# Optimization experiments

Measured on AMD Instinct MI355X. Metric: run time of the kernel, lower is better.

Reference implementation:

```python
import jax, jax.numpy as jnp
import numpy as np

EPS = 1e-8
VOX_WIDTH = 1.0
CURV_THRESH = 0.5


def _build_kernels():
    """Nine 3x3x3 central finite-difference stencils, pre-divided by vox_width / vox_width^2."""
    def zk():
        return np.zeros((3, 3, 3), np.float32)
    ks = {}
    # first derivatives (central difference), denominator vox_width
    for name, ax in (('ddx', 0), ('ddy', 1), ('ddz', 2)):
        k = zk(); i = [1, 1, 1]
        i[ax] = 0; k[tuple(i)] = -0.5
        i[ax] = 2; k[tuple(i)] = 0.5
        ks[name] = k / VOX_WIDTH
    # pure second derivatives, denominator vox_width^2
    for name, ax in (('d2dx2', 0), ('d2dy2', 1), ('d2dz2', 2)):
        k = zk(); i = [1, 1, 1]
        i[ax] = 0; k[tuple(i)] = 1.0
        i[ax] = 1; k[tuple(i)] = -2.0
        i[ax] = 2; k[tuple(i)] = 1.0
        ks[name] = k / VOX_WIDTH ** 2
    # mixed second derivatives, denominator vox_width^2
    for name, (a, b) in (('d2dxdy', (0, 1)), ('d2dxdz', (0, 2)), ('d2dydz', (1, 2))):
        k = zk()
        for sa, sb, v in ((0, 0, 0.25), (0, 2, -0.25), (2, 0, -0.25), (2, 2, 0.25)):
            i = [1, 1, 1]; i[a] = sa; i[b] = sb; k[tuple(i)] = v
        ks[name] = k / VOX_WIDTH ** 2
    order = ['ddx', 'ddy', 'ddz', 'd2dx2', 'd2dy2', 'd2dz2', 'd2dxdy', 'd2dxdz', 'd2dydz']
    return np.stack([ks[n] for n in order])[:, None]  # [9, 1, 3, 3, 3]


_KERNELS = jnp.asarray(_build_kernels())


def setup_inputs() -> dict:
    key = jax.random.key(0)
    phi = jax.random.normal(key, (2, 1, 192, 192, 192), dtype=jnp.float32)
    return {"phi": phi}


def reference(phi):
    # all nine stencils as one valid 3D conv: [N, 9, D-2, H-2, W-2]
    g = jax.lax.conv_general_dilated(
        phi, _KERNELS, window_strides=(1, 1, 1), padding='VALID',
        dimension_numbers=('NCDHW', 'OIDHW', 'NCDHW'))
    gx, gy, gz, hxx, hyy, hzz, hxy, hxz, hyz = (g[:, i:i + 1] for i in range(9))

    mag = jnp.sqrt(gx * gx + gy * gy + gz * gz + EPS)
    mag3 = mag ** 3

    # mean curvature: sum_{i!=j} g_i^2 H_jj - 2 sum_{i<j} g_i g_j H_ij, over |grad|^3
    cross = gx * gy * hxy + gx * gz * hxz + gy * gz * hyz
    mean_c = (gx * gx * (hyy + hzz) + gy * gy * (hxx + hzz) + gz * gz * (hxx + hyy)
              - 2.0 * cross) / (mag3 + EPS)

    # gaussian curvature: laplacian/|grad| - (g^T H g)/|grad|^3
    lap = (hxx + hyy + hzz) / (mag + EPS)
    quad = (gx * gx * hxx + gy * gy * hyy + gz * gz * hzz + 2.0 * cross) / (mag3 + EPS)
    gauss = lap - quad

    k1 = mean_c + jnp.sqrt(jnp.abs(mean_c ** 2 - gauss) + EPS)
    pen = jax.nn.relu((k1 / (CURV_THRESH + EPS)) ** 2 - 1.0)

    # zero crossings of phi over 3x3x3 neighborhoods (valid -> matches conv output shape)
    mn = jax.lax.reduce_window(phi, jnp.inf, jax.lax.min, (1, 1, 3, 3, 3), (1, 1, 1, 1, 1), 'VALID')
    mx = jax.lax.reduce_window(phi, -jnp.inf, jax.lax.max, (1, 1, 3, 3, 3), (1, 1, 1, 1, 1), 'VALID')
    phi_zero = jax.lax.stop_gradient((mn * mx < 0).astype(phi.dtype))

    return jnp.sum(phi_zero * pen) / (jnp.sum(phi_zero) + EPS)
```

## Files before the change

### kernel.cpp

```cpp
#include <hip/hip_runtime.h>


typedef float v2f __attribute__((ext_vector_type(2)));

constexpr int DIM  = 192;
constexpr int ODIM = 190;
constexpr int TX = 32, TY = 32, CZ = 19;
constexpr int NTX = 6, NTY = 6, NTZ = 10;
constexpr int PLANE = DIM * DIM;
constexpr int NBLOCKS = 2 * NTZ * NTY * NTX;

struct Slice {
    v2f   q[3][4];
    float xmn[4], xmx[4];
};

__global__ __launch_bounds__(256, 3) void curv_main(const float* __restrict__ phi,
                                                    double* __restrict__ acc,
                                                    int use_partials) {
    int bx = blockIdx.x;
    const int tx = bx % NTX; bx /= NTX;
    const int ty = bx % NTY; bx /= NTY;
    const int tz = bx % NTZ; bx /= NTZ;
    const int n  = bx;

    const int xbase = tx * TX, ybase = ty * TY, zbase = tz * CZ;
    const int tid = threadIdx.x;
    const int row = tid >> 3;
    const int x0  = (tid & 7) * 4;
    const float* pn = phi + (long long)n * DIM * PLANE;

    const int c4 = xbase + x0;
    int c2t = c4 + 4; if (c2t > DIM - 2) c2t = DIM - 2;
    const int c2 = c2t;
    int yoff[3];
#pragma unroll
    for (int dy = 0; dy < 3; ++dy) {
        int iy = ybase + row + dy; if (iy > DIM - 1) iy = DIM - 1;
        yoff[dy] = iy * DIM;
    }

    float4 t4[3]; float2 t2[3];
    auto pref = [&](int g) {
        const float* base = pn + (zbase + g) * PLANE;
#pragma unroll
        for (int dy = 0; dy < 3; ++dy) {
            t4[dy] = *(const float4*)(base + yoff[dy] + c4);
            t2[dy] = *(const float2*)(base + yoff[dy] + c2);
        }
    };

    auto unpack = [&](Slice& s) {
        float mn6[6], mx6[6];
#pragma unroll
        for (int dy = 0; dy < 3; ++dy) {
            const float4 a = t4[dy]; const float2 b = t2[dy];
            s.q[dy][0] = (v2f){a.x, a.z};
            s.q[dy][1] = (v2f){a.y, a.w};
            s.q[dy][2] = (v2f){a.z, b.x};
            s.q[dy][3] = (v2f){a.w, b.y};
            if (dy == 0) {
                mn6[0] = a.x; mn6[1] = a.y; mn6[2] = a.z;
                mn6[3] = a.w; mn6[4] = b.x; mn6[5] = b.y;
                mx6[0] = a.x; mx6[1] = a.y; mx6[2] = a.z;
                mx6[3] = a.w; mx6[4] = b.x; mx6[5] = b.y;
            } else {
                mn6[0] = fminf(mn6[0], a.x); mx6[0] = fmaxf(mx6[0], a.x);
                mn6[1] = fminf(mn6[1], a.y); mx6[1] = fmaxf(mx6[1], a.y);
                mn6[2] = fminf(mn6[2], a.z); mx6[2] = fmaxf(mx6[2], a.z);
                mn6[3] = fminf(mn6[3], a.w); mx6[3] = fmaxf(mx6[3], a.w);
                mn6[4] = fminf(mn6[4], b.x); mx6[4] = fmaxf(mx6[4], b.x);
                mn6[5] = fminf(mn6[5], b.y); mx6[5] = fmaxf(mx6[5], b.y);
            }
        }
#pragma unroll
        for (int j = 0; j < 4; ++j) {
            s.xmn[j] = fminf(fminf(mn6[j], mn6[j + 1]), mn6[j + 2]);
            s.xmx[j] = fmaxf(fmaxf(mx6[j], mx6[j + 1]), mx6[j + 2]);
        }
    };

    float fsp = 0.0f, fsc = 0.0f;
    const float EPSF = 1e-8f;
    const float EPS4 = 4e-8f;
    const int oy = ybase + row;

    bool vmask[4];
#pragma unroll
    for (int j = 0; j < 4; ++j)
        vmask[j] = (oy < ODIM) && (xbase + x0 + j < ODIM);

    auto compute = [&](const Slice& s0, const Slice& s1, const Slice& s2) {
        float wmn[4], wmx[4];
#pragma unroll
        for (int j = 0; j < 4; ++j) {
            wmn[j] = fminf(fminf(s0.xmn[j], s1.xmn[j]), s2.xmn[j]);
            wmx[j] = fmaxf(fmaxf(s0.xmx[j], s1.xmx[j]), s2.xmx[j]);
        }

#pragma unroll
        for (int p = 0; p < 2; ++p) {
            v2f Gx = s2.q[1][p + 1] - s0.q[1][p + 1];
            v2f Gy = s1.q[2][p + 1] - s1.q[0][p + 1];
            v2f Gz = s1.q[1][p + 2] - s1.q[1][p];

            v2f c2v = 2.0f * s1.q[1][p + 1];
            v2f hxx = s0.q[1][p + 1] - c2v + s2.q[1][p + 1];
            v2f hyy = s1.q[0][p + 1] - c2v + s1.q[2][p + 1];
            v2f hzz = s1.q[1][p] - c2v + s1.q[1][p + 2];

            v2f Mxy = s0.q[0][p + 1] - s0.q[2][p + 1]
                    - s2.q[0][p + 1] + s2.q[2][p + 1];
            v2f Mxz = s0.q[1][p] - s0.q[1][p + 2]
                    - s2.q[1][p] + s2.q[1][p + 2];
            v2f Myz = s1.q[0][p] - s1.q[0][p + 2]
                    - s1.q[2][p] + s1.q[2][p + 2];

            v2f Gx2 = Gx * Gx, Gy2 = Gy * Gy, Gz2 = Gz * Gz;
            v2f mag2G = Gx2 + Gy2 + Gz2 + EPS4;

            v2f r = (v2f){ __builtin_amdgcn_rsqf(mag2G.x),
                           __builtin_amdgcn_rsqf(mag2G.y) };
            v2f r3 = r * r * r;
            v2f twor3 = r3 + r3;

            v2f crossG = Gx * Gy * Mxy + Gx * Gz * Mxz + Gy * Gz * Myz;

            v2f num1 = Gx2 * (hyy + hzz) + Gy2 * (hxx + hzz) +
                       Gz2 * (hxx + hyy) - 0.5f * crossG;
            v2f mean_c = num1 * twor3;
            v2f lap   = (hxx + hyy + hzz) * (r + r);
            v2f num2  = Gx2 * hxx + Gy2 * hyy + Gz2 * hzz + 0.5f * crossG;
            v2f quad  = num2 * twor3;
            v2f gauss = lap - quad;

            v2f disc = mean_c * mean_c - gauss;
            v2f sq = (v2f){ sqrtf(fabsf(disc.x) + EPSF),
                            sqrtf(fabsf(disc.y) + EPSF) };
            v2f k1 = mean_c + sq;
            v2f t  = 2.0f * k1;
            v2f pen2 = t * t - 1.0f;

#pragma unroll
            for (int e = 0; e < 2; ++e) {
                const int j = p + 2 * e;
                float pen = fmaxf(e ? pen2.y : pen2.x, 0.0f);
                if (vmask[j] && (wmn[j] * wmx[j] < 0.0f)) {
                    fsp += pen;
                    fsc += 1.0f;
                }
            }
        }
    };

    Slice s0, s1, s2;

    pref(0); unpack(s0);
    pref(1); unpack(s1);
    pref(2);

    unpack(s2); pref(3);  compute(s0, s1, s2);
    unpack(s0); pref(4);  compute(s1, s2, s0);
    unpack(s1); pref(5);  compute(s2, s0, s1);
    unpack(s2); pref(6);  compute(s0, s1, s2);
    unpack(s0); pref(7);  compute(s1, s2, s0);
    unpack(s1); pref(8);  compute(s2, s0, s1);
    unpack(s2); pref(9);  compute(s0, s1, s2);
    unpack(s0); pref(10); compute(s1, s2, s0);
    unpack(s1); pref(11); compute(s2, s0, s1);
    unpack(s2); pref(12); compute(s0, s1, s2);
    unpack(s0); pref(13); compute(s1, s2, s0);
    unpack(s1); pref(14); compute(s2, s0, s1);
    unpack(s2); pref(15); compute(s0, s1, s2);
    unpack(s0); pref(16); compute(s1, s2, s0);
    unpack(s1); pref(17); compute(s2, s0, s1);
    unpack(s2); pref(18); compute(s0, s1, s2);
    unpack(s0); pref(19); compute(s1, s2, s0);
    unpack(s1); pref(20); compute(s2, s0, s1);
    unpack(s2);           compute(s0, s1, s2);

    double sp = (double)fsp, sc = (double)fsc;
#pragma unroll
    for (int off = 32; off > 0; off >>= 1) {
        sp += __shfl_down(sp, off, 64);
        sc += __shfl_down(sc, off, 64);
    }

    __shared__ double lsp[4], lsc[4];
    const int wave = tid >> 6, lane = tid & 63;
    if (lane == 0) { lsp[wave] = sp; lsc[wave] = sc; }
    __syncthreads();
    if (tid == 0) {
        double tp = lsp[0] + lsp[1] + lsp[2] + lsp[3];
        double tc = lsc[0] + lsc[1] + lsc[2] + lsc[3];
        if (use_partials) {
            acc[2 * blockIdx.x]     = tp;
            acc[2 * blockIdx.x + 1] = tc;
        } else {
            atomicAdd(&acc[0], tp);
            atomicAdd(&acc[1], tc);
        }
    }
}

__global__ __launch_bounds__(256) void curv_reduce(const double* __restrict__ part,
                                                   int nblocks, int use_partials,
                                                   float* __restrict__ out) {
    double sp = 0.0, sc = 0.0;
    if (use_partials) {
        for (int i = threadIdx.x; i < nblocks; i += 256) {
            sp += part[2 * i];
            sc += part[2 * i + 1];
        }
    } else if (threadIdx.x == 0) {
        sp = part[0]; sc = part[1];
    }
#pragma unroll
    for (int off = 32; off > 0; off >>= 1) {
        sp += __shfl_down(sp, off, 64);
        sc += __shfl_down(sc, off, 64);
    }
    __shared__ double lsp[4], lsc[4];
    const int wave = threadIdx.x >> 6, lane = threadIdx.x & 63;
    if (lane == 0) { lsp[wave] = sp; lsc[wave] = sc; }
    __syncthreads();
    if (threadIdx.x == 0) {
        double tp = lsp[0] + lsp[1] + lsp[2] + lsp[3];
        double tc = lsc[0] + lsc[1] + lsc[2] + lsc[3];
        out[0] = (float)(tp / (tc + 1e-8));
    }
}

extern "C" void kernel_launch(void* const* d_in, const int* in_sizes, int n_in,
                              void* d_out, int out_size, void* d_ws, size_t ws_size,
                              hipStream_t stream) {
    const float* phi = (const float*)d_in[0];
    float* out = (float*)d_out;
    double* acc = (double*)d_ws;

    const int use_partials = (ws_size >= (size_t)(2 * NBLOCKS) * sizeof(double)) ? 1 : 0;
    if (!use_partials) {
        hipMemsetAsync(d_ws, 0, 2 * sizeof(double), stream);
    }

    curv_main<<<NBLOCKS, 256, 0, stream>>>(phi, acc, use_partials);
    curv_reduce<<<1, 256, 0, stream>>>(acc, NBLOCKS, use_partials, out);
}
```

Baseline: 108.4 us.

## Fuse final reduction via last-block ticket, double-buffer prefetch, compact slice registers

The separate reduction kernel is replaced by a last-block-done pattern: each block writes its partial, bumps an atomic ticket, and the final block reduces all partials and writes the output. Launching one fewer kernel removes the launch gap, but a memset for the ticket is added. Prefetch now uses two alternating register buffers, so loads are issued two z-planes ahead. Slice storage is compacted from 12 to 9 packed pairs per slice, rebuilding the shifted pairs on demand to cut register pressure.

```diff
diff --git a/kernel.cpp b/kernel.cpp
--- a/kernel.cpp
+++ b/kernel.cpp
@@ -10,14 +10,53 @@
 constexpr int PLANE = DIM * DIM;
 constexpr int NBLOCKS = 2 * NTZ * NTY * NTX;
 
+struct Row { v2f A, B, C; };
 struct Slice {
-    v2f   q[3][4];
+    Row   r[3];
     float xmn[4], xmx[4];
 };
 
+#define PREF(T4, T2, g) do {                                             \
+    const float* base_ = pn + (zbase + (g)) * PLANE;                     \
+    _Pragma("unroll")                                                    \
+    for (int dy = 0; dy < 3; ++dy) {                                     \
+        T4[dy] = *(const float4*)(base_ + yoff[dy] + c4);                \
+        T2[dy] = *(const float2*)(base_ + yoff[dy] + c2);                \
+    } } while (0)
+
+#define UNPACK(S, T4, T2) do {                                           \
+    float mn6[6], mx6[6];                                                \
+    _Pragma("unroll")                                                    \
+    for (int dy = 0; dy < 3; ++dy) {                                     \
+        const float4 a = T4[dy]; const float2 b = T2[dy];                \
+        (S).r[dy].A = (v2f){a.x, a.z};                                   \
+        (S).r[dy].B = (v2f){a.y, a.w};                                   \
+        (S).r[dy].C = (v2f){b.x, b.y};                                   \
+        if (dy == 0) {                                                   \
+            mn6[0] = a.x; mn6[1] = a.y; mn6[2] = a.z;                    \
+            mn6[3] = a.w; mn6[4] = b.x; mn6[5] = b.y;                    \
+            mx6[0] = a.x; mx6[1] = a.y; mx6[2] = a.z;                    \
+            mx6[3] = a.w; mx6[4] = b.x; mx6[5] = b.y;                    \
+        } else {                                                         \
+            mn6[0] = fminf(mn6[0], a.x); mx6[0] = fmaxf(mx6[0], a.x);    \
+            mn6[1] = fminf(mn6[1], a.y); mx6[1] = fmaxf(mx6[1], a.y);    \
+            mn6[2] = fminf(mn6[2], a.z); mx6[2] = fmaxf(mx6[2], a.z);    \
+            mn6[3] = fminf(mn6[3], a.w); mx6[3] = fmaxf(mx6[3], a.w);    \
+            mn6[4] = fminf(mn6[4], b.x); mx6[4] = fmaxf(mx6[4], b.x);    \
+            mn6[5] = fminf(mn6[5], b.y); mx6[5] = fmaxf(mx6[5], b.y);    \
+        }                                                                \
+    }                                                                    \
+    _Pragma("unroll")                                                    \
+    for (int j = 0; j < 4; ++j) {                                        \
+        (S).xmn[j] = fminf(fminf(mn6[j], mn6[j + 1]), mn6[j + 2]);       \
+        (S).xmx[j] = fmaxf(fmaxf(mx6[j], mx6[j + 1]), mx6[j + 2]);       \
+    } } while (0)
+
 __global__ __launch_bounds__(256, 3) void curv_main(const float* __restrict__ phi,
                                                     double* __restrict__ acc,
-                                                    int use_partials) {
+                                                    float* __restrict__ out,
+                                                    unsigned* __restrict__ ticket,
+                                                    int mode) {
     int bx = blockIdx.x;
     const int tx = bx % NTX; bx /= NTX;
     const int ty = bx % NTY; bx /= NTY;
@@ -40,45 +79,8 @@
         yoff[dy] = iy * DIM;
     }
 
-    float4 t4[3]; float2 t2[3];
-    auto pref = [&](int g) {
-        const float* base = pn + (zbase + g) * PLANE;
-#pragma unroll
-        for (int dy = 0; dy < 3; ++dy) {
-            t4[dy] = *(const float4*)(base + yoff[dy] + c4);
-            t2[dy] = *(const float2*)(base + yoff[dy] + c2);
-        }
-    };
-
-    auto unpack = [&](Slice& s) {
-        float mn6[6], mx6[6];
-#pragma unroll
-        for (int dy = 0; dy < 3; ++dy) {
-            const float4 a = t4[dy]; const float2 b = t2[dy];
-            s.q[dy][0] = (v2f){a.x, a.z};
-            s.q[dy][1] = (v2f){a.y, a.w};
-            s.q[dy][2] = (v2f){a.z, b.x};
-            s.q[dy][3] = (v2f){a.w, b.y};
-            if (dy == 0) {
-                mn6[0] = a.x; mn6[1] = a.y; mn6[2] = a.z;
-                mn6[3] = a.w; mn6[4] = b.x; mn6[5] = b.y;
-                mx6[0] = a.x; mx6[1] = a.y; mx6[2] = a.z;
-                mx6[3] = a.w; mx6[4] = b.x; mx6[5] = b.y;
-            } else {
-                mn6[0] = fminf(mn6[0], a.x); mx6[0] = fmaxf(mx6[0], a.x);
-                mn6[1] = fminf(mn6[1], a.y); mx6[1] = fmaxf(mx6[1], a.y);
-                mn6[2] = fminf(mn6[2], a.z); mx6[2] = fmaxf(mx6[2], a.z);
-                mn6[3] = fminf(mn6[3], a.w); mx6[3] = fmaxf(mx6[3], a.w);
-                mn6[4] = fminf(mn6[4], b.x); mx6[4] = fmaxf(mx6[4], b.x);
-                mn6[5] = fminf(mn6[5], b.y); mx6[5] = fmaxf(mx6[5], b.y);
-            }
-        }
-#pragma unroll
-        for (int j = 0; j < 4; ++j) {
-            s.xmn[j] = fminf(fminf(mn6[j], mn6[j + 1]), mn6[j + 2]);
-            s.xmx[j] = fmaxf(fmaxf(mx6[j], mx6[j + 1]), mx6[j + 2]);
-        }
-    };
+    float4 tA4[3]; float2 tA2[3];
+    float4 tB4[3]; float2 tB2[3];
 
     float fsp = 0.0f, fsc = 0.0f;
     const float EPSF = 1e-8f;
@@ -90,6 +92,13 @@
     for (int j = 0; j < 4; ++j)
         vmask[j] = (oy < ODIM) && (xbase + x0 + j < ODIM);
 
+    auto PK = [](const Row& w, int k) -> v2f {
+        return k == 0 ? w.A
+             : (k == 1 ? w.B
+             : (k == 2 ? (v2f){w.A.y, w.C.x}
+                       : (v2f){w.B.y, w.C.y}));
+    };
+
     auto compute = [&](const Slice& s0, const Slice& s1, const Slice& s2) {
         float wmn[4], wmx[4];
 #pragma unroll
@@ -100,21 +109,29 @@
 
 #pragma unroll
         for (int p = 0; p < 2; ++p) {
-            v2f Gx = s2.q[1][p + 1] - s0.q[1][p + 1];
-            v2f Gy = s1.q[2][p + 1] - s1.q[0][p + 1];
-            v2f Gz = s1.q[1][p + 2] - s1.q[1][p];
-
-            v2f c2v = 2.0f * s1.q[1][p + 1];
-            v2f hxx = s0.q[1][p + 1] - c2v + s2.q[1][p + 1];
-            v2f hyy = s1.q[0][p + 1] - c2v + s1.q[2][p + 1];
-            v2f hzz = s1.q[1][p] - c2v + s1.q[1][p + 2];
-
-            v2f Mxy = s0.q[0][p + 1] - s0.q[2][p + 1]
-                    - s2.q[0][p + 1] + s2.q[2][p + 1];
-            v2f Mxz = s0.q[1][p] - s0.q[1][p + 2]
-                    - s2.q[1][p] + s2.q[1][p + 2];
-            v2f Myz = s1.q[0][p] - s1.q[0][p + 2]
-                    - s1.q[2][p] + s1.q[2][p + 2];
+            const v2f a0 = PK(s0.r[1], p + 1);
+            const v2f a2 = PK(s2.r[1], p + 1);
+            const v2f b0 = PK(s1.r[0], p + 1);
+            const v2f b2 = PK(s1.r[2], p + 1);
+            const v2f cc = PK(s1.r[1], p + 1);
+            const v2f zm = PK(s1.r[1], p);
+            const v2f zp = PK(s1.r[1], p + 2);
+
+            v2f Gx = a2 - a0;
+            v2f Gy = b2 - b0;
+            v2f Gz = zp - zm;
+
+            v2f c2v = 2.0f * cc;
+            v2f hxx = a0 - c2v + a2;
+            v2f hyy = b0 - c2v + b2;
+            v2f hzz = zm - c2v + zp;
+
+            v2f Mxy = PK(s0.r[0], p + 1) - PK(s0.r[2], p + 1)
+                    - PK(s2.r[0], p + 1) + PK(s2.r[2], p + 1);
+            v2f Mxz = PK(s0.r[1], p) - PK(s0.r[1], p + 2)
+                    - PK(s2.r[1], p) + PK(s2.r[1], p + 2);
+            v2f Myz = PK(s1.r[0], p) - PK(s1.r[0], p + 2)
+                    - PK(s1.r[2], p) + PK(s1.r[2], p + 2);
 
             v2f Gx2 = Gx * Gx, Gy2 = Gy * Gy, Gz2 = Gz * Gz;
             v2f mag2G = Gx2 + Gy2 + Gz2 + EPS4;
@@ -155,29 +172,29 @@
 
     Slice s0, s1, s2;
 
-    pref(0); unpack(s0);
-    pref(1); unpack(s1);
-    pref(2);
-
-    unpack(s2); pref(3);  compute(s0, s1, s2);
-    unpack(s0); pref(4);  compute(s1, s2, s0);
-    unpack(s1); pref(5);  compute(s2, s0, s1);
-    unpack(s2); pref(6);  compute(s0, s1, s2);
-    unpack(s0); pref(7);  compute(s1, s2, s0);
-    unpack(s1); pref(8);  compute(s2, s0, s1);
-    unpack(s2); pref(9);  compute(s0, s1, s2);
-    unpack(s0); pref(10); compute(s1, s2, s0);
-    unpack(s1); pref(11); compute(s2, s0, s1);
-    unpack(s2); pref(12); compute(s0, s1, s2);
-    unpack(s0); pref(13); compute(s1, s2, s0);
-    unpack(s1); pref(14); compute(s2, s0, s1);
-    unpack(s2); pref(15); compute(s0, s1, s2);
-    unpack(s0); pref(16); compute(s1, s2, s0);
-    unpack(s1); pref(17); compute(s2, s0, s1);
-    unpack(s2); pref(18); compute(s0, s1, s2);
-    unpack(s0); pref(19); compute(s1, s2, s0);
-    unpack(s1); pref(20); compute(s2, s0, s1);
-    unpack(s2);           compute(s0, s1, s2);
+    PREF(tA4, tA2, 0); PREF(tB4, tB2, 1);
+    UNPACK(s0, tA4, tA2); PREF(tA4, tA2, 2);
+    UNPACK(s1, tB4, tB2); PREF(tB4, tB2, 3);
+
+    UNPACK(s2, tA4, tA2); PREF(tA4, tA2, 4);  compute(s0, s1, s2);
+    UNPACK(s0, tB4, tB2); PREF(tB4, tB2, 5);  compute(s1, s2, s0);
+    UNPACK(s1, tA4, tA2); PREF(tA4, tA2, 6);  compute(s2, s0, s1);
+    UNPACK(s2, tB4, tB2); PREF(tB4, tB2, 7);  compute(s0, s1, s2);
+    UNPACK(s0, tA4, tA2); PREF(tA4, tA2, 8);  compute(s1, s2, s0);
+    UNPACK(s1, tB4, tB2); PREF(tB4, tB2, 9);  compute(s2, s0, s1);
+    UNPACK(s2, tA4, tA2); PREF(tA4, tA2, 10); compute(s0, s1, s2);
+    UNPACK(s0, tB4, tB2); PREF(tB4, tB2, 11); compute(s1, s2, s0);
+    UNPACK(s1, tA4, tA2); PREF(tA4, tA2, 12); compute(s2, s0, s1);
+    UNPACK(s2, tB4, tB2); PREF(tB4, tB2, 13); compute(s0, s1, s2);
+    UNPACK(s0, tA4, tA2); PREF(tA4, tA2, 14); compute(s1, s2, s0);
+    UNPACK(s1, tB4, tB2); PREF(tB4, tB2, 15); compute(s2, s0, s1);
+    UNPACK(s2, tA4, tA2); PREF(tA4, tA2, 16); compute(s0, s1, s2);
+    UNPACK(s0, tB4, tB2); PREF(tB4, tB2, 17); compute(s1, s2, s0);
+    UNPACK(s1, tA4, tA2); PREF(tA4, tA2, 18); compute(s2, s0, s1);
+    UNPACK(s2, tB4, tB2); PREF(tB4, tB2, 19); compute(s0, s1, s2);
+    UNPACK(s0, tA4, tA2); PREF(tA4, tA2, 20); compute(s1, s2, s0);
+    UNPACK(s1, tB4, tB2);                     compute(s2, s0, s1);
+    UNPACK(s2, tA4, tA2);                     compute(s0, s1, s2);
 
     double sp = (double)fsp, sc = (double)fsc;
 #pragma unroll
@@ -187,48 +204,53 @@
     }
 
     __shared__ double lsp[4], lsc[4];
+    __shared__ int is_last;
     const int wave = tid >> 6, lane = tid & 63;
     if (lane == 0) { lsp[wave] = sp; lsc[wave] = sc; }
     __syncthreads();
     if (tid == 0) {
         double tp = lsp[0] + lsp[1] + lsp[2] + lsp[3];
         double tc = lsc[0] + lsc[1] + lsc[2] + lsc[3];
-        if (use_partials) {
+        if (mode) {
             acc[2 * blockIdx.x]     = tp;
             acc[2 * blockIdx.x + 1] = tc;
+            __threadfence();
+            unsigned prev = atomicAdd(ticket, 1u);
+            is_last = (prev == (unsigned)(NBLOCKS - 1)) ? 1 : 0;
         } else {
             atomicAdd(&acc[0], tp);
             atomicAdd(&acc[1], tc);
+            is_last = 0;
+        }
+    }
+    __syncthreads();
+
+    if (is_last) {
+        __threadfence();
+        double rp = 0.0, rc = 0.0;
+        for (int i = tid; i < NBLOCKS; i += 256) {
+            rp += acc[2 * i];
+            rc += acc[2 * i + 1];
+        }
+#pragma unroll
+        for (int off = 32; off > 0; off >>= 1) {
+            rp += __shfl_down(rp, off, 64);
+            rc += __shfl_down(rc, off, 64);
+        }
+        if (lane == 0) { lsp[wave] = rp; lsc[wave] = rc; }
+        __syncthreads();
+        if (tid == 0) {
+            double tp = lsp[0] + lsp[1] + lsp[2] + lsp[3];
+            double tc = lsc[0] + lsc[1] + lsc[2] + lsc[3];
+            out[0] = (float)(tp / (tc + 1e-8));
         }
     }
 }
 
-__global__ __launch_bounds__(256) void curv_reduce(const double* __restrict__ part,
-                                                   int nblocks, int use_partials,
-                                                   float* __restrict__ out) {
-    double sp = 0.0, sc = 0.0;
-    if (use_partials) {
-        for (int i = threadIdx.x; i < nblocks; i += 256) {
-            sp += part[2 * i];
-            sc += part[2 * i + 1];
-        }
-    } else if (threadIdx.x == 0) {
-        sp = part[0]; sc = part[1];
-    }
-#pragma unroll
-    for (int off = 32; off > 0; off >>= 1) {
-        sp += __shfl_down(sp, off, 64);
-        sc += __shfl_down(sc, off, 64);
-    }
-    __shared__ double lsp[4], lsc[4];
-    const int wave = threadIdx.x >> 6, lane = threadIdx.x & 63;
-    if (lane == 0) { lsp[wave] = sp; lsc[wave] = sc; }
-    __syncthreads();
-    if (threadIdx.x == 0) {
-        double tp = lsp[0] + lsp[1] + lsp[2] + lsp[3];
-        double tc = lsc[0] + lsc[1] + lsc[2] + lsc[3];
-        out[0] = (float)(tp / (tc + 1e-8));
-    }
+__global__ void curv_reduce(const double* __restrict__ acc,
+                            float* __restrict__ out) {
+    if (threadIdx.x == 0)
+        out[0] = (float)(acc[0] / (acc[1] + 1e-8));
 }
 
 extern "C" void kernel_launch(void* const* d_in, const int* in_sizes, int n_in,
@@ -238,11 +260,14 @@
     float* out = (float*)d_out;
     double* acc = (double*)d_ws;
 
-    const int use_partials = (ws_size >= (size_t)(2 * NBLOCKS) * sizeof(double)) ? 1 : 0;
-    if (!use_partials) {
+    const size_t need = (size_t)(2 * NBLOCKS) * sizeof(double) + sizeof(unsigned);
+    if (ws_size >= need) {
+        unsigned* ticket = (unsigned*)(acc + 2 * NBLOCKS);
+        hipMemsetAsync(ticket, 0, sizeof(unsigned), stream);
+        curv_main<<<NBLOCKS, 256, 0, stream>>>(phi, acc, out, ticket, 1);
+    } else {
         hipMemsetAsync(d_ws, 0, 2 * sizeof(double), stream);
-    }
-
-    curv_main<<<NBLOCKS, 256, 0, stream>>>(phi, acc, use_partials);
-    curv_reduce<<<1, 256, 0, stream>>>(acc, NBLOCKS, use_partials, out);
+        curv_main<<<NBLOCKS, 256, 0, stream>>>(phi, acc, out, (unsigned*)nullptr, 0);
+        curv_reduce<<<1, 256, 0, stream>>>(acc, out);
+    }
 }
```

Result: slower. 121.7 us (+12.2%).
